# Optimization experiments

Hardware: AMD Instinct MI355X
Metric: run time of the kernel (lower is better)

Reference implementation:

```python
import jax, jax.numpy as jnp
import numpy as np

B, L, D, H = 8, 1024, 1024, 16
DH = D // H  # dim_per_head = 64
HG = H // 2  # global/local head split


def setup_inputs() -> dict:
    key = jax.random.key(0)
    ks = jax.random.split(key, 10)
    s = 1.0 / np.sqrt(D)
    return {
        "key": jax.random.normal(ks[0], (B, L, D), jnp.float32),
        "value": jax.random.normal(ks[1], (B, L, D), jnp.float32),
        "query": jax.random.normal(ks[2], (B, L, D), jnp.float32),
        "mask": jax.random.bernoulli(ks[3], 0.1, (B, L, L)),
        "additional_mask": jax.random.bernoulli(ks[4], 0.1, (B, L)),
        "Wk": jax.random.normal(ks[5], (D, D), jnp.float32) * s,
        "bk": jnp.zeros((D,), jnp.float32),
        "Wv": jax.random.normal(ks[6], (D, D), jnp.float32) * s,
        "bv": jnp.zeros((D,), jnp.float32),
        "Wq": jax.random.normal(ks[7], (D, D), jnp.float32) * s,
        "bq": jnp.zeros((D,), jnp.float32),
        "Wo": jax.random.normal(ks[8], (D, D), jnp.float32) * s,
        "bo": jnp.zeros((D,), jnp.float32),
    }


def _shape(x):
    # [B, L, D] -> [B, H, L, DH]
    return x.reshape(B, -1, H, DH).transpose(0, 2, 1, 3)


def reference(key, value, query, mask, additional_mask,
              Wk, bk, Wv, bv, Wq, bq, Wo, bo):
    # projections (torch Linear: x @ W.T + b)
    k = _shape(key @ Wk.T + bk)
    v = _shape(value @ Wv.T + bv)
    q = _shape(query @ Wq.T + bq) * (1.0 / np.sqrt(DH))  # scale query (edge_feature=None, additional_mask given)

    qg, ql = q[:, :HG], q[:, HG:]
    kg, kl = k[:, :HG], k[:, HG:]
    vg, vl = v[:, :HG], v[:, HG:]

    # global heads: standard masked attention
    score_g = jnp.einsum('bhqd,bhkd->bhqk', qg, kg)
    top_score = score_g[:, 0]  # taken BEFORE masking, as in original
    score_g = jnp.where(mask[:, None, :, :], -1e18, score_g)
    attn_g = jax.nn.softmax(score_g, axis=-1)  # dropout = identity (eval)
    ctx_g = jnp.einsum('bhqk,bhkd->bhqd', attn_g, vg)

    # local heads: additional_mask [B, k] broadcast over heads and queries
    score_l = jnp.einsum('bhqd,bhkd->bhqk', ql, kl)
    score_l = jnp.where(additional_mask[:, None, None, :], -1e18, score_l)
    attn_l = jax.nn.softmax(score_l, axis=-1)
    ctx_l = jnp.einsum('bhqk,bhkd->bhqd', attn_l, vl)

    ctx = jnp.concatenate([ctx_g, ctx_l], axis=1)          # [B, H, L, DH]
    ctx = ctx.transpose(0, 2, 1, 3).reshape(B, -1, D)      # unshape -> [B, L, D]
    out = ctx @ Wo.T + bo
    return out, top_score
```

## Files before the change

kernel.cpp:

```cpp
#include <hip/hip_runtime.h>
#include <hip/hip_bf16.h>

typedef unsigned short u16;
typedef unsigned int u32;
typedef __attribute__((ext_vector_type(8))) short short8;
typedef __attribute__((ext_vector_type(4))) short short4v;
typedef __attribute__((ext_vector_type(4))) float floatx4;

#define BB 8
#define LL 1024
#define DD 1024
#define HH 16
#define DHH 64
#define NEGBIG (-3.0e38f)

__device__ inline u16 f2b(float f) {
  union { __hip_bfloat16 h; u16 u; } cv;
  cv.h = __float2bfloat16(f);
  return cv.u;
}
__device__ inline float b2f(u16 u) {
  union { u16 u; __hip_bfloat16 h; } cv;
  cv.u = u;
  return __bfloat162float(cv.h);
}
__device__ inline float fin(float v, float sentinel) {
  return (fabsf(v) < 1e30f) ? v : sentinel;
}
__device__ inline void async16(const void* g, void* l) {
  __builtin_amdgcn_global_load_lds(
      (__attribute__((address_space(1))) void*)(const_cast<void*>(g)),
      (__attribute__((address_space(3))) void*)l, 16, 0, 0);
}


__global__ __launch_bounds__(256) void convpack(
    const float* __restrict__ key, const float* __restrict__ value,
    const float* __restrict__ query, const float* __restrict__ Wk,
    const float* __restrict__ Wv, const float* __restrict__ Wq,
    const float* __restrict__ Wo, const int* __restrict__ mask,
    const int* __restrict__ amask, u16* __restrict__ keyb,
    u16* __restrict__ valb, u16* __restrict__ qryb, u16* __restrict__ Wkb,
    u16* __restrict__ Wvb, u16* __restrict__ Wqb, u16* __restrict__ Wob,
    u32* __restrict__ maskb, u32* __restrict__ amaskb) {
  const int job = blockIdx.y;
  const int gtid = blockIdx.x * 256 + threadIdx.x;
  const int stride = gridDim.x * 256;

  if (job < 7) {
    const float* src; u16* dst; size_t n4;
    switch (job) {
      case 0: src = key;   dst = keyb; n4 = (size_t)BB * LL * DD / 4; break;
      case 1: src = value; dst = valb; n4 = (size_t)BB * LL * DD / 4; break;
      case 2: src = query; dst = qryb; n4 = (size_t)BB * LL * DD / 4; break;
      case 3: src = Wk;    dst = Wkb;  n4 = (size_t)DD * DD / 4; break;
      case 4: src = Wv;    dst = Wvb;  n4 = (size_t)DD * DD / 4; break;
      case 5: src = Wq;    dst = Wqb;  n4 = (size_t)DD * DD / 4; break;
      default: src = Wo;   dst = Wob;  n4 = (size_t)DD * DD / 4; break;
    }
    for (size_t i = gtid; i < n4; i += stride) {
      float4 v = ((const float4*)src)[i];
      short4v s;
      s[0] = (short)f2b(v.x); s[1] = (short)f2b(v.y);
      s[2] = (short)f2b(v.z); s[3] = (short)f2b(v.w);
      *(short4v*)(dst + i * 4) = s;
    }
  } else if (job == 7) {
    const size_t nw = (size_t)BB * LL * LL / 32;
    for (size_t w = gtid; w < nw; w += stride) {
      const int4* src = (const int4*)(mask + w * 32);
      u32 bits = 0;
#pragma unroll
      for (int c = 0; c < 8; c++) {
        int4 v = src[c];
        bits |= (u32)(v.x != 0) << (c * 4);
        bits |= (u32)(v.y != 0) << (c * 4 + 1);
        bits |= (u32)(v.z != 0) << (c * 4 + 2);
        bits |= (u32)(v.w != 0) << (c * 4 + 3);
      }
      maskb[w] = bits;
    }
  } else {
    const int nw = BB * LL / 32;
    for (int w = gtid; w < nw; w += stride) {
      const int4* src = (const int4*)(amask + w * 32);
      u32 bits = 0;
#pragma unroll
      for (int c = 0; c < 8; c++) {
        int4 v = src[c];
        bits |= (u32)(v.x != 0) << (c * 4);
        bits |= (u32)(v.y != 0) << (c * 4 + 1);
        bits |= (u32)(v.z != 0) << (c * 4 + 2);
        bits |= (u32)(v.w != 0) << (c * 4 + 3);
      }
      amaskb[w] = bits;
    }
  }
}

template <int OUT>
__global__ __launch_bounds__(256) void gemm_b(
    const u16* __restrict__ A, const u16* __restrict__ Wb,
    const float* __restrict__ bias, void* __restrict__ outv, float scale) {
  __shared__ u16 As[128 * 32];
  __shared__ u16 Ws[128 * 32];

  const int tid = threadIdx.x;
  const int wave = tid >> 6, lane = tid & 63;
  const int lr = lane & 15, lq = lane >> 4;
  const int row0 = blockIdx.x * 128;
  const int col0 = blockIdx.y * 128;
  const int wm = (wave & 1) * 64, wn = (wave >> 1) * 64;

  floatx4 acc[4][4];
#pragma unroll
  for (int i = 0; i < 4; i++)
#pragma unroll
    for (int j = 0; j < 4; j++) acc[i][j] = (floatx4){0.f, 0.f, 0.f, 0.f};

  const int cc0 = tid, cc1 = 256 + tid;
  const u16* Ag0 = A + (size_t)(row0 + (cc0 >> 2)) * 1024 + (cc0 & 3) * 8;
  const u16* Ag1 = A + (size_t)(row0 + (cc1 >> 2)) * 1024 + (cc1 & 3) * 8;
  const u16* Wg0 = Wb + (size_t)(col0 + (cc0 >> 2)) * 1024 + (cc0 & 3) * 8;
  const u16* Wg1 = Wb + (size_t)(col0 + (cc1 >> 2)) * 1024 + (cc1 & 3) * 8;
  u16* As0 = As + wave * 512;
  u16* As1 = As + 2048 + wave * 512;
  u16* Ws0 = Ws + wave * 512;
  u16* Ws1 = Ws + 2048 + wave * 512;

  for (int k0 = 0; k0 < 1024; k0 += 32) {
    __syncthreads();
    async16(Ag0 + k0, As0);
    async16(Ag1 + k0, As1);
    async16(Wg0 + k0, Ws0);
    async16(Wg1 + k0, Ws1);
    __syncthreads();

    short8 af[4], wf[4];
#pragma unroll
    for (int mi = 0; mi < 4; mi++)
      af[mi] = *(const short8*)(As + (wm + mi * 16 + lr) * 32 + lq * 8);
#pragma unroll
    for (int ni = 0; ni < 4; ni++)
      wf[ni] = *(const short8*)(Ws + (wn + ni * 16 + lr) * 32 + lq * 8);
#pragma unroll
    for (int mi = 0; mi < 4; mi++)
#pragma unroll
      for (int ni = 0; ni < 4; ni++)
        acc[mi][ni] = __builtin_amdgcn_mfma_f32_16x16x32_bf16(af[mi], wf[ni],
                                                              acc[mi][ni], 0, 0, 0);
  }

#pragma unroll
  for (int ni = 0; ni < 4; ni++) {
    const int col = col0 + wn + ni * 16 + lr;
    const float bv = bias[col];
#pragma unroll
    for (int mi = 0; mi < 4; mi++) {
#pragma unroll
      for (int r = 0; r < 4; r++) {
        const int row = row0 + wm + mi * 16 + lq * 4 + r;
        const float v = (acc[mi][ni][r] + bv) * scale;
        if (OUT == 0) {
          const int b = row >> 10, l = row & 1023, h = col >> 6, dh = col & 63;
          ((u16*)outv)[((b * HH + h) * LL + l) * DHH + dh] = f2b(v);
        } else if (OUT == 2) {
          const int b = row >> 10, l = row & 1023, h = col >> 6, dh = col & 63;
          ((u16*)outv)[((b * HH + h) * DHH + dh) * LL + l] = f2b(v);
        } else {
          ((float*)outv)[(size_t)row * 1024 + col] = v;
        }
      }
    }
  }
}

__global__ __launch_bounds__(256) void attn_fast(
    const u16* __restrict__ qbuf, const u16* __restrict__ kbuf,
    const u16* __restrict__ vbt, const u32* __restrict__ maskb,
    const u32* __restrict__ amaskb, u16* __restrict__ ctx,
    float* __restrict__ top) {
  __shared__ u16 Ks[64 * 64];
  __shared__ u16 Vts[64 * 64];

  const int id = blockIdx.x;
  const int xcd = id & 7;
  const int r_ = id >> 3;
  const int b = r_ & 7;
  const int h = (((r_ >> 3) & 1) << 3) | (xcd ^ b);
  const int qt = r_ >> 4;

  const int tid = threadIdx.x, wave = tid >> 6, lane = tid & 63;
  const int lr = lane & 15, lq = lane >> 4;
  const int lq4 = lq * 4;
  const int x7 = lr & 7;

  const u16* Qg = qbuf + (size_t)((b * HH + h) * LL + qt * 128) * DHH;
  const u16* Kg = kbuf + (size_t)((b * HH + h) * LL) * DHH;
  const u16* Vtg = vbt + (size_t)((b * HH + h) * DHH) * LL;

  short8 qf[2][2];
#pragma unroll
  for (int mi = 0; mi < 2; mi++)
#pragma unroll
    for (int kk = 0; kk < 2; kk++)
      qf[mi][kk] = *(const short8*)(Qg + (wave * 32 + mi * 16 + lr) * 64 +
                                    kk * 32 + lq * 8);

  const int g0 = tid, g1 = 256 + tid;
  const int kr0 = g0 >> 3, kc0 = (g0 & 7) ^ (kr0 & 7);
  const int kr1 = g1 >> 3, kc1 = (g1 & 7) ^ (kr1 & 7);
  const int cs0 = ((0 + lq) ^ x7) * 8;
  const int cs1 = ((4 + lq) ^ x7) * 8;
  const int lqh = lq >> 1, lqb = (lq & 1) * 4;
  const int go00 = ((0 + lqh) ^ x7) * 8 + lqb;
  const int go01 = ((2 + lqh) ^ x7) * 8 + lqb;
  const int go10 = ((4 + lqh) ^ x7) * 8 + lqb;
  const int go11 = ((6 + lqh) ^ x7) * 8 + lqb;

  float mrow[2], lrow[2];
  floatx4 Oacc[2][4];
#pragma unroll
  for (int mi = 0; mi < 2; mi++) {
    mrow[mi] = NEGBIG;
    lrow[mi] = 0.f;
#pragma unroll
    for (int ni = 0; ni < 4; ni++) Oacc[mi][ni] = (floatx4){0.f, 0.f, 0.f, 0.f};
  }

  for (int kc = 0; kc < 16; kc++) {
    __syncthreads();
    async16(Kg + kc * 4096 + kr0 * 64 + kc0 * 8, Ks + wave * 512);
    async16(Kg + kc * 4096 + kr1 * 64 + kc1 * 8, Ks + 2048 + wave * 512);
    async16(Vtg + (size_t)kr0 * LL + kc * 64 + kc0 * 8, Vts + wave * 512);
    async16(Vtg + (size_t)kr1 * LL + kc * 64 + kc1 * 8, Vts + 2048 + wave * 512);
    __syncthreads();

    floatx4 S[2][4];
#pragma unroll
    for (int nj = 0; nj < 4; nj++) {
      const short8 kf0 = *(const short8*)(Ks + (nj * 16 + lr) * 64 + cs0);
      const short8 kf1 = *(const short8*)(Ks + (nj * 16 + lr) * 64 + cs1);
#pragma unroll
      for (int mi = 0; mi < 2; mi++) {
        floatx4 z = (floatx4){0.f, 0.f, 0.f, 0.f};
        z = __builtin_amdgcn_mfma_f32_16x16x32_bf16(kf1, qf[mi][1], z, 0, 0, 0);
        z = __builtin_amdgcn_mfma_f32_16x16x32_bf16(kf0, qf[mi][0], z, 0, 0, 0);
        S[mi][nj] = z;
      }
    }

    short8 pf[2][2];
#pragma unroll
    for (int mi = 0; mi < 2; mi++) {
      const int row = qt * 128 + wave * 32 + mi * 16 + lr;

      if (h == 0) {
        float* tp = top + (size_t)(b * LL + row) * LL + kc * 64 + lq4;
#pragma unroll
        for (int nj = 0; nj < 4; nj++) {
          float4 t;
          t.x = S[mi][nj][0]; t.y = S[mi][nj][1];
          t.z = S[mi][nj][2]; t.w = S[mi][nj][3];
          *(float4*)(tp + nj * 16) = t;
        }
      }

      if (h < 8) {
        const uint2 mw =
            *(const uint2*)(maskb + (size_t)(b * LL + row) * 32 + kc * 2);
#pragma unroll
        for (int nj = 0; nj < 4; nj++) {
          const u32 nib = (((nj & 2) ? mw.y : mw.x) >> ((nj & 1) * 16 + lq4)) & 15u;
#pragma unroll
          for (int r = 0; r < 4; r++)
            if ((nib >> r) & 1) S[mi][nj][r] = -1e18f;
        }
      } else {
        const uint2 aw = *(const uint2*)(amaskb + b * 32 + kc * 2);
#pragma unroll
        for (int nj = 0; nj < 4; nj++) {
          const u32 nib = (((nj & 2) ? aw.y : aw.x) >> ((nj & 1) * 16 + lq4)) & 15u;
#pragma unroll
          for (int r = 0; r < 4; r++)
            if ((nib >> r) & 1) S[mi][nj][r] = -1e18f;
        }
      }

      float cm = fmaxf(fmaxf(S[mi][0][0], S[mi][0][1]),
                       fmaxf(S[mi][0][2], S[mi][0][3]));
#pragma unroll
      for (int nj = 1; nj < 4; nj++)
        cm = fmaxf(cm, fmaxf(fmaxf(S[mi][nj][0], S[mi][nj][1]),
                             fmaxf(S[mi][nj][2], S[mi][nj][3])));
      cm = fmaxf(cm, __shfl_xor(cm, 16, 64));
      cm = fmaxf(cm, __shfl_xor(cm, 32, 64));
      const float mold = mrow[mi];
      const float mnew = fmaxf(mold, cm);
      const float alpha = __expf(mold - mnew);
      mrow[mi] = mnew;
      float rs = 0.f;
#pragma unroll
      for (int nj = 0; nj < 4; nj++)
#pragma unroll
        for (int r = 0; r < 4; r++) {
          const float p = __expf(S[mi][nj][r] - mnew);
          S[mi][nj][r] = p;
          rs += p;
        }
      rs += __shfl_xor(rs, 16, 64);
      rs += __shfl_xor(rs, 32, 64);
      lrow[mi] = lrow[mi] * alpha + rs;
#pragma unroll
      for (int ni = 0; ni < 4; ni++)
#pragma unroll
        for (int r = 0; r < 4; r++) Oacc[mi][ni][r] *= alpha;

#pragma unroll
      for (int kk = 0; kk < 2; kk++) {
        short8 p;
#pragma unroll
        for (int r = 0; r < 4; r++) {
          p[r] = (short)f2b(S[mi][2 * kk][r]);
          p[4 + r] = (short)f2b(S[mi][2 * kk + 1][r]);
        }
        pf[mi][kk] = p;
      }
    }

#pragma unroll
    for (int ni = 0; ni < 4; ni++) {
      const int rb = (ni * 16 + lr) * 64;
      const short4v v00 = *(const short4v*)(Vts + rb + go00);
      const short4v v01 = *(const short4v*)(Vts + rb + go01);
      const short4v v10 = *(const short4v*)(Vts + rb + go10);
      const short4v v11 = *(const short4v*)(Vts + rb + go11);
      const short8 vf0 = __builtin_shufflevector(v00, v01, 0, 1, 2, 3, 4, 5, 6, 7);
      const short8 vf1 = __builtin_shufflevector(v10, v11, 0, 1, 2, 3, 4, 5, 6, 7);
#pragma unroll
      for (int mi = 0; mi < 2; mi++) {
        Oacc[mi][ni] =
            __builtin_amdgcn_mfma_f32_16x16x32_bf16(vf0, pf[mi][0], Oacc[mi][ni], 0, 0, 0);
        Oacc[mi][ni] =
            __builtin_amdgcn_mfma_f32_16x16x32_bf16(vf1, pf[mi][1], Oacc[mi][ni], 0, 0, 0);
      }
    }
  }

#pragma unroll
  for (int mi = 0; mi < 2; mi++) {
    const float inv = 1.0f / lrow[mi];
    const int row = qt * 128 + wave * 32 + mi * 16 + lr;
    u16* cp = ctx + (size_t)(b * LL + row) * DD + h * DHH + lq4;
#pragma unroll
    for (int ni = 0; ni < 4; ni++) {
      short4v o;
      o[0] = (short)f2b(Oacc[mi][ni][0] * inv);
      o[1] = (short)f2b(Oacc[mi][ni][1] * inv);
      o[2] = (short)f2b(Oacc[mi][ni][2] * inv);
      o[3] = (short)f2b(Oacc[mi][ni][3] * inv);
      *(short4v*)(cp + ni * 16) = o;
    }
  }
}

template <int MODE>
__global__ __launch_bounds__(256) void gemm_k(
    const void* __restrict__ Av, const float* __restrict__ W,
    const float* __restrict__ biasp, void* __restrict__ outv, float scale) {
  __shared__ u16 As[128 * 32];
  __shared__ u16 Ws[128 * 32];
  const int tid = threadIdx.x;
  const int wave = tid >> 6, lane = tid & 63;
  const int lr = lane & 15, lq = lane >> 4;
  const int row0 = blockIdx.x * 128;
  const int col0 = blockIdx.y * 128;
  const int wm = (wave & 1) * 64, wn = (wave >> 1) * 64;
  floatx4 acc[4][4];
#pragma unroll
  for (int i = 0; i < 4; i++)
#pragma unroll
    for (int j = 0; j < 4; j++) acc[i][j] = (floatx4){0.f, 0.f, 0.f, 0.f};
  const float* Af = (const float*)Av;
  const u16* Ab = (const u16*)Av;
  for (int k0 = 0; k0 < 1024; k0 += 32) {
    float4 wg[4];
#pragma unroll
    for (int it = 0; it < 4; it++) {
      const int cc = it * 256 + tid;
      wg[it] = *(const float4*)(W + (size_t)(col0 + (cc >> 3)) * 1024 + (cc & 7) * 4 + k0);
    }
    float4 ag[4];
    short8 ab0, ab1;
    if (MODE == 0) {
#pragma unroll
      for (int it = 0; it < 4; it++) {
        const int cc = it * 256 + tid;
        ag[it] = *(const float4*)(Af + (size_t)(row0 + (cc >> 3)) * 1024 + (cc & 7) * 4 + k0);
      }
    } else {
      const int cc0 = tid, cc1 = 256 + tid;
      ab0 = *(const short8*)(Ab + (size_t)(row0 + (cc0 >> 2)) * 1024 + (cc0 & 3) * 8 + k0);
      ab1 = *(const short8*)(Ab + (size_t)(row0 + (cc1 >> 2)) * 1024 + (cc1 & 3) * 8 + k0);
    }
    __syncthreads();
#pragma unroll
    for (int it = 0; it < 4; it++) {
      const int cc = it * 256 + tid;
      short4v s;
      s[0] = (short)f2b(wg[it].x); s[1] = (short)f2b(wg[it].y);
      s[2] = (short)f2b(wg[it].z); s[3] = (short)f2b(wg[it].w);
      *(short4v*)(Ws + (cc >> 3) * 32 + (cc & 7) * 4) = s;
    }
    if (MODE == 0) {
#pragma unroll
      for (int it = 0; it < 4; it++) {
        const int cc = it * 256 + tid;
        short4v s;
        s[0] = (short)f2b(ag[it].x); s[1] = (short)f2b(ag[it].y);
        s[2] = (short)f2b(ag[it].z); s[3] = (short)f2b(ag[it].w);
        *(short4v*)(As + (cc >> 3) * 32 + (cc & 7) * 4) = s;
      }
    } else {
      *(short8*)(As + tid * 8) = ab0;
      *(short8*)(As + (256 + tid) * 8) = ab1;
    }
    __syncthreads();
    short8 af[4], wf[4];
#pragma unroll
    for (int mi = 0; mi < 4; mi++)
      af[mi] = *(const short8*)(As + (wm + mi * 16 + lr) * 32 + lq * 8);
#pragma unroll
    for (int ni = 0; ni < 4; ni++)
      wf[ni] = *(const short8*)(Ws + (wn + ni * 16 + lr) * 32 + lq * 8);
#pragma unroll
    for (int mi = 0; mi < 4; mi++)
#pragma unroll
      for (int ni = 0; ni < 4; ni++)
        acc[mi][ni] = __builtin_amdgcn_mfma_f32_16x16x32_bf16(af[mi], wf[ni], acc[mi][ni], 0, 0, 0);
  }
#pragma unroll
  for (int ni = 0; ni < 4; ni++) {
    const int col = col0 + wn + ni * 16 + lr;
    const float bv = biasp[col];
#pragma unroll
    for (int mi = 0; mi < 4; mi++) {
#pragma unroll
      for (int r = 0; r < 4; r++) {
        const int row = row0 + wm + mi * 16 + lq * 4 + r;
        float v = (acc[mi][ni][r] + bv) * scale;
        v = fin(v, MODE == 0 ? 700.0f : 1000.0f);
        if (MODE == 0) {
          const int b = row >> 10, l = row & 1023, h = col >> 6, dh = col & 63;
          ((u16*)outv)[((b * HH + h) * LL + l) * DHH + dh] = f2b(v);
        } else {
          ((float*)outv)[(size_t)row * 1024 + col] = v;
        }
      }
    }
  }
}

__global__ __launch_bounds__(256) void attn_kernel(
    const u16* __restrict__ qbuf, const u16* __restrict__ kbuf,
    const u16* __restrict__ vbuf, const int* __restrict__ mask,
    const int* __restrict__ amask, u16* __restrict__ ctx,
    float* __restrict__ top) {
  __shared__ u16 Qs[128 * 64];
  __shared__ u16 Ks[64 * 64];
  __shared__ u16 Vts[64 * 64];
  __shared__ u16 Ps[4][32 * 64];
  const int qt = blockIdx.x, h = blockIdx.y, b = blockIdx.z;
  const int tid = threadIdx.x, wave = tid >> 6, lane = tid & 63;
  const int lr = lane & 15, lq = lane >> 4;
  const u16* Qg = qbuf + (size_t)((b * HH + h) * LL + qt * 128) * DHH;
  const u16* Kg = kbuf + (size_t)((b * HH + h) * LL) * DHH;
  const u16* Vg = vbuf + (size_t)((b * HH + h) * LL) * DHH;
#pragma unroll
  for (int it = 0; it < 4; it++) {
    short8 qv = *(const short8*)(Qg + (it * 256 + tid) * 8);
    *(short8*)(Qs + (it * 256 + tid) * 8) = qv;
  }
  float mrow[2][4], lrow[2][4];
  floatx4 Oacc[2][4];
#pragma unroll
  for (int mi = 0; mi < 2; mi++)
#pragma unroll
    for (int r = 0; r < 4; r++) { mrow[mi][r] = NEGBIG; lrow[mi][r] = 0.f; }
#pragma unroll
  for (int mi = 0; mi < 2; mi++)
#pragma unroll
    for (int ni = 0; ni < 4; ni++) Oacc[mi][ni] = (floatx4){0.f, 0.f, 0.f, 0.f};
  for (int kc = 0; kc < 16; kc++) {
    const u16* Kc = Kg + kc * 64 * DHH;
    const u16* Vc = Vg + kc * 64 * DHH;
    short8 kv0 = *(const short8*)(Kc + tid * 8);
    short8 kv1 = *(const short8*)(Kc + (256 + tid) * 8);
    short8 vv0 = *(const short8*)(Vc + tid * 8);
    short8 vv1 = *(const short8*)(Vc + (256 + tid) * 8);
    __syncthreads();
    *(short8*)(Ks + tid * 8) = kv0;
    *(short8*)(Ks + (256 + tid) * 8) = kv1;
    {
      const int r0 = tid >> 3, e0 = (tid & 7) * 8;
#pragma unroll
      for (int j = 0; j < 8; j++) Vts[(e0 + j) * 64 + r0] = (u16)vv0[j];
      const int cc1 = 256 + tid;
      const int r1 = cc1 >> 3, e1 = (cc1 & 7) * 8;
#pragma unroll
      for (int j = 0; j < 8; j++) Vts[(e1 + j) * 64 + r1] = (u16)vv1[j];
    }
    __syncthreads();
    floatx4 S[2][4];
    short8 qf[2][2];
#pragma unroll
    for (int mi = 0; mi < 2; mi++)
#pragma unroll
      for (int kk = 0; kk < 2; kk++)
        qf[mi][kk] = *(const short8*)(Qs + (wave * 32 + mi * 16 + lr) * 64 + kk * 32 + lq * 8);
#pragma unroll
    for (int nj = 0; nj < 4; nj++) {
      short8 kf0 = *(const short8*)(Ks + (nj * 16 + lr) * 64 + lq * 8);
      short8 kf1 = *(const short8*)(Ks + (nj * 16 + lr) * 64 + 32 + lq * 8);
#pragma unroll
      for (int mi = 0; mi < 2; mi++) {
        floatx4 z = (floatx4){0.f, 0.f, 0.f, 0.f};
        z = __builtin_amdgcn_mfma_f32_16x16x32_bf16(qf[mi][1], kf1, z, 0, 0, 0);
        z = __builtin_amdgcn_mfma_f32_16x16x32_bf16(qf[mi][0], kf0, z, 0, 0, 0);
        S[mi][nj] = z;
      }
    }
#pragma unroll
    for (int mi = 0; mi < 2; mi++)
#pragma unroll
      for (int nj = 0; nj < 4; nj++)
#pragma unroll
        for (int r = 0; r < 4; r++) S[mi][nj][r] = fin(S[mi][nj][r], 800.0f);
    if (h == 0) {
#pragma unroll
      for (int mi = 0; mi < 2; mi++)
#pragma unroll
        for (int nj = 0; nj < 4; nj++)
#pragma unroll
          for (int r = 0; r < 4; r++) {
            const int row = qt * 128 + wave * 32 + mi * 16 + lq * 4 + r;
            const int colk = kc * 64 + nj * 16 + lr;
            top[(size_t)(b * LL + row) * LL + colk] = S[mi][nj][r];
          }
    }
    if (h < 8) {
#pragma unroll
      for (int mi = 0; mi < 2; mi++)
#pragma unroll
        for (int r = 0; r < 4; r++) {
          const int row = qt * 128 + wave * 32 + mi * 16 + lq * 4 + r;
          const int* mp = mask + (size_t)(b * LL + row) * LL + kc * 64;
#pragma unroll
          for (int nj = 0; nj < 4; nj++) {
            const int mv = mp[nj * 16 + lr];
            S[mi][nj][r] = mv ? -1e18f : S[mi][nj][r];
          }
        }
    } else {
#pragma unroll
      for (int nj = 0; nj < 4; nj++) {
        const int mv = amask[b * LL + kc * 64 + nj * 16 + lr];
        if (mv) {
#pragma unroll
          for (int mi = 0; mi < 2; mi++)
#pragma unroll
            for (int r = 0; r < 4; r++) S[mi][nj][r] = -1e18f;
        }
      }
    }
#pragma unroll
    for (int mi = 0; mi < 2; mi++) {
#pragma unroll
      for (int r = 0; r < 4; r++) {
        float cm = S[mi][0][r];
#pragma unroll
        for (int nj = 1; nj < 4; nj++) cm = fmaxf(cm, S[mi][nj][r]);
#pragma unroll
        for (int off = 1; off < 16; off <<= 1) cm = fmaxf(cm, __shfl_xor(cm, off, 64));
        const float mold = mrow[mi][r];
        const float mnew = fmaxf(mold, cm);
        const float alpha = __expf(mold - mnew);
        mrow[mi][r] = mnew;
        float rs = 0.f;
#pragma unroll
        for (int nj = 0; nj < 4; nj++) {
          const float p = __expf(S[mi][nj][r] - mnew);
          S[mi][nj][r] = p;
          rs += p;
        }
#pragma unroll
        for (int off = 1; off < 16; off <<= 1) rs += __shfl_xor(rs, off, 64);
        lrow[mi][r] = lrow[mi][r] * alpha + rs;
#pragma unroll
        for (int ni = 0; ni < 4; ni++) Oacc[mi][ni][r] *= alpha;
      }
    }
#pragma unroll
    for (int mi = 0; mi < 2; mi++)
#pragma unroll
      for (int nj = 0; nj < 4; nj++)
#pragma unroll
        for (int r = 0; r < 4; r++)
          Ps[wave][(mi * 16 + lq * 4 + r) * 64 + nj * 16 + lr] = f2b(S[mi][nj][r]);
    __syncthreads();
#pragma unroll
    for (int kk = 0; kk < 2; kk++) {
      short8 pf[2];
#pragma unroll
      for (int mi = 0; mi < 2; mi++)
        pf[mi] = *(const short8*)(&Ps[wave][(mi * 16 + lr) * 64 + kk * 32 + lq * 8]);
#pragma unroll
      for (int ni = 0; ni < 4; ni++) {
        short8 vf = *(const short8*)(Vts + (ni * 16 + lr) * 64 + kk * 32 + lq * 8);
#pragma unroll
        for (int mi = 0; mi < 2; mi++)
          Oacc[mi][ni] = __builtin_amdgcn_mfma_f32_16x16x32_bf16(pf[mi], vf, Oacc[mi][ni], 0, 0, 0);
      }
    }
  }
#pragma unroll
  for (int mi = 0; mi < 2; mi++)
#pragma unroll
    for (int r = 0; r < 4; r++) {
      const float inv = 1.0f / lrow[mi][r];
      const int row = qt * 128 + wave * 32 + mi * 16 + lq * 4 + r;
#pragma unroll
      for (int ni = 0; ni < 4; ni++) {
        const int col = h * DHH + ni * 16 + lr;
        ctx[(size_t)(b * LL + row) * DD + col] = f2b(fin(Oacc[mi][ni][r] * inv, 900.0f));
      }
    }
}

extern "C" void kernel_launch(void* const* d_in, const int* in_sizes, int n_in,
                              void* d_out, int out_size, void* d_ws, size_t ws_size,
                              hipStream_t stream) {
  const float* key   = (const float*)d_in[0];
  const float* value = (const float*)d_in[1];
  const float* query = (const float*)d_in[2];
  const int* mask    = (const int*)d_in[3];
  const int* amask   = (const int*)d_in[4];
  const float* Wk = (const float*)d_in[5];
  const float* bk = (const float*)d_in[6];
  const float* Wv = (const float*)d_in[7];
  const float* bv = (const float*)d_in[8];
  const float* Wq = (const float*)d_in[9];
  const float* bq = (const float*)d_in[10];
  const float* Wo = (const float*)d_in[11];
  const float* bo = (const float*)d_in[12];

  float* outp = (float*)d_out;
  float* topp = outp + (size_t)BB * LL * DD;

  const size_t M8 = (size_t)BB * LL * DD;
  const size_t M1 = (size_t)DD * DD;
  const size_t NEED = (size_t)90 * 1024 * 1024;

  dim3 tb(256), gg(64, 8, 1), ga(8, 16, 8);

  if (ws_size >= NEED) {
    u16* W16 = (u16*)d_ws;
    u16* keyb = W16;
    u16* valb = W16 + M8;
    u16* qryb = W16 + 2 * M8;
    u16* Wkb = W16 + 3 * M8;
    u16* Wvb = Wkb + M1;
    u16* Wqb = Wvb + M1;
    u16* Wob = Wqb + M1;
    u32* maskb = (u32*)(Wob + M1);
    u32* amaskb = maskb + 262144;
    u16* kbuf = W16 + 3 * M8 + 5 * M1;
    u16* vbt  = kbuf + M8;
    u16* qbuf = keyb;
    u16* cbuf = valb;

    convpack<<<dim3(256, 9), tb, 0, stream>>>(
        key, value, query, Wk, Wv, Wq, Wo, mask, amask,
        keyb, valb, qryb, Wkb, Wvb, Wqb, Wob, maskb, amaskb);
    gemm_b<0><<<gg, tb, 0, stream>>>(keyb, Wkb, bk, kbuf, 1.0f);
    gemm_b<2><<<gg, tb, 0, stream>>>(valb, Wvb, bv, vbt, 1.0f);
    gemm_b<0><<<gg, tb, 0, stream>>>(qryb, Wqb, bq, qbuf, 0.125f);
    attn_fast<<<dim3(1024, 1, 1), tb, 0, stream>>>(qbuf, kbuf, vbt, maskb,
                                                   amaskb, cbuf, topp);
    gemm_b<1><<<gg, tb, 0, stream>>>(cbuf, Wob, bo, outp, 1.0f);
  } else {
    u16* kbuf = (u16*)d_ws;
    u16* vbuf = kbuf + M8;
    u16* qbuf = vbuf + M8;
    u16* cbuf = qbuf + M8;
    gemm_k<0><<<gg, tb, 0, stream>>>(key,   Wk, bk, kbuf, 1.0f);
    gemm_k<0><<<gg, tb, 0, stream>>>(value, Wv, bv, vbuf, 1.0f);
    gemm_k<0><<<gg, tb, 0, stream>>>(query, Wq, bq, qbuf, 0.125f);
    attn_kernel<<<ga, tb, 0, stream>>>(qbuf, kbuf, vbuf, mask, amask, cbuf, topp);
    gemm_k<1><<<gg, tb, 0, stream>>>(cbuf, Wo, bo, outp, 1.0f);
  }
}
```

Baseline: 421.6 us.

## Fuse QKV projections with in-kernel query cast; double-buffer attention and use exp2

Replaces the three separate Q/K/V projection launches with one 3D-grid GEMM launch. The query branch reads fp32 activations and casts them to bf16 inside the GEMM, which removes the separate query conversion pass and its buffer. The attention kernel now double-buffers the K/V tiles in LDS, so the next chunk's loads overlap compute, and raises wave priority around the MFMA sections. The softmax uses exp2, with log2(e) folded into the query scale and the pre-mask top score rescaled by ln2. The trade-offs are doubled LDS in attention and a query GEMM path that issues register-staged global loads inside the k-loop.

New measurement: 428.4 us. No clear change (+1.6%).

```diff
diff --git a/kernel.cpp b/kernel.cpp
--- a/kernel.cpp
+++ b/kernel.cpp
@@ -13,6 +13,8 @@
 #define HH 16
 #define DHH 64
 #define NEGBIG (-3.0e38f)
+#define QSCALE 0.1803368801111204f
+#define LN2F   0.6931471805599453f
 
 __device__ inline u16 f2b(float f) {
   union { __hip_bfloat16 h; u16 u; } cv;
@@ -27,6 +29,13 @@
 __device__ inline float fin(float v, float sentinel) {
   return (fabsf(v) < 1e30f) ? v : sentinel;
 }
+__device__ inline float fexp2(float x) {
+#if __has_builtin(__builtin_amdgcn_exp2f)
+  return __builtin_amdgcn_exp2f(x);
+#else
+  return exp2f(x);
+#endif
+}
 __device__ inline void async16(const void* g, void* l) {
   __builtin_amdgcn_global_load_lds(
       (__attribute__((address_space(1))) void*)(const_cast<void*>(g)),
@@ -36,26 +45,24 @@
 
 __global__ __launch_bounds__(256) void convpack(
     const float* __restrict__ key, const float* __restrict__ value,
-    const float* __restrict__ query, const float* __restrict__ Wk,
-    const float* __restrict__ Wv, const float* __restrict__ Wq,
-    const float* __restrict__ Wo, const int* __restrict__ mask,
-    const int* __restrict__ amask, u16* __restrict__ keyb,
-    u16* __restrict__ valb, u16* __restrict__ qryb, u16* __restrict__ Wkb,
+    const float* __restrict__ Wk, const float* __restrict__ Wv,
+    const float* __restrict__ Wq, const float* __restrict__ Wo,
+    const int* __restrict__ mask, const int* __restrict__ amask,
+    u16* __restrict__ keyb, u16* __restrict__ valb, u16* __restrict__ Wkb,
     u16* __restrict__ Wvb, u16* __restrict__ Wqb, u16* __restrict__ Wob,
     u32* __restrict__ maskb, u32* __restrict__ amaskb) {
   const int job = blockIdx.y;
   const int gtid = blockIdx.x * 256 + threadIdx.x;
   const int stride = gridDim.x * 256;
 
-  if (job < 7) {
+  if (job < 6) {
     const float* src; u16* dst; size_t n4;
     switch (job) {
       case 0: src = key;   dst = keyb; n4 = (size_t)BB * LL * DD / 4; break;
       case 1: src = value; dst = valb; n4 = (size_t)BB * LL * DD / 4; break;
-      case 2: src = query; dst = qryb; n4 = (size_t)BB * LL * DD / 4; break;
-      case 3: src = Wk;    dst = Wkb;  n4 = (size_t)DD * DD / 4; break;
-      case 4: src = Wv;    dst = Wvb;  n4 = (size_t)DD * DD / 4; break;
-      case 5: src = Wq;    dst = Wqb;  n4 = (size_t)DD * DD / 4; break;
+      case 2: src = Wk;    dst = Wkb;  n4 = (size_t)DD * DD / 4; break;
+      case 3: src = Wv;    dst = Wvb;  n4 = (size_t)DD * DD / 4; break;
+      case 4: src = Wq;    dst = Wqb;  n4 = (size_t)DD * DD / 4; break;
       default: src = Wo;   dst = Wob;  n4 = (size_t)DD * DD / 4; break;
     }
     for (size_t i = gtid; i < n4; i += stride) {
@@ -65,7 +72,7 @@
       s[2] = (short)f2b(v.z); s[3] = (short)f2b(v.w);
       *(short4v*)(dst + i * 4) = s;
     }
-  } else if (job == 7) {
+  } else if (job == 6) {
     const size_t nw = (size_t)BB * LL * LL / 32;
     for (size_t w = gtid; w < nw; w += stride) {
       const int4* src = (const int4*)(mask + w * 32);
@@ -94,6 +101,131 @@
         bits |= (u32)(v.w != 0) << (c * 4 + 3);
       }
       amaskb[w] = bits;
+    }
+  }
+}
+
+__global__ __launch_bounds__(256) void gemm_qkv(
+    const u16* __restrict__ keyb, const u16* __restrict__ valb,
+    const float* __restrict__ query, const u16* __restrict__ Wkb,
+    const u16* __restrict__ Wvb, const u16* __restrict__ Wqb,
+    const float* __restrict__ bk, const float* __restrict__ bv,
+    const float* __restrict__ bq, u16* __restrict__ kbuf,
+    u16* __restrict__ vbt, u16* __restrict__ qbuf) {
+  __shared__ u16 As[128 * 32];
+  __shared__ u16 Ws[128 * 32];
+
+  const int z = blockIdx.z;
+  const int tid = threadIdx.x;
+  const int wave = tid >> 6, lane = tid & 63;
+  const int lr = lane & 15, lq = lane >> 4;
+  const int row0 = blockIdx.x * 128;
+  const int col0 = blockIdx.y * 128;
+  const int wm = (wave & 1) * 64, wn = (wave >> 1) * 64;
+
+  floatx4 acc[4][4];
+#pragma unroll
+  for (int i = 0; i < 4; i++)
+#pragma unroll
+    for (int j = 0; j < 4; j++) acc[i][j] = (floatx4){0.f, 0.f, 0.f, 0.f};
+
+  const int cc0 = tid, cc1 = 256 + tid;
+  u16* As0 = As + wave * 512;
+  u16* As1 = As + 2048 + wave * 512;
+  u16* Ws0 = Ws + wave * 512;
+  u16* Ws1 = Ws + 2048 + wave * 512;
+
+  if (z < 2) {
+    const u16* A  = (z == 0) ? keyb : valb;
+    const u16* Wb = (z == 0) ? Wkb : Wvb;
+    const u16* Ag0 = A + (size_t)(row0 + (cc0 >> 2)) * 1024 + (cc0 & 3) * 8;
+    const u16* Ag1 = A + (size_t)(row0 + (cc1 >> 2)) * 1024 + (cc1 & 3) * 8;
+    const u16* Wg0 = Wb + (size_t)(col0 + (cc0 >> 2)) * 1024 + (cc0 & 3) * 8;
+    const u16* Wg1 = Wb + (size_t)(col0 + (cc1 >> 2)) * 1024 + (cc1 & 3) * 8;
+
+    for (int k0 = 0; k0 < 1024; k0 += 32) {
+      __syncthreads();
+      async16(Ag0 + k0, As0);
+      async16(Ag1 + k0, As1);
+      async16(Wg0 + k0, Ws0);
+      async16(Wg1 + k0, Ws1);
+      __syncthreads();
+
+      short8 af[4], wf[4];
+#pragma unroll
+      for (int mi = 0; mi < 4; mi++)
+        af[mi] = *(const short8*)(As + (wm + mi * 16 + lr) * 32 + lq * 8);
+#pragma unroll
+      for (int ni = 0; ni < 4; ni++)
+        wf[ni] = *(const short8*)(Ws + (wn + ni * 16 + lr) * 32 + lq * 8);
+#pragma unroll
+      for (int mi = 0; mi < 4; mi++)
+#pragma unroll
+        for (int ni = 0; ni < 4; ni++)
+          acc[mi][ni] = __builtin_amdgcn_mfma_f32_16x16x32_bf16(af[mi], wf[ni],
+                                                                acc[mi][ni], 0, 0, 0);
+    }
+  } else {
+    const u16* Wg0 = Wqb + (size_t)(col0 + (cc0 >> 2)) * 1024 + (cc0 & 3) * 8;
+    const u16* Wg1 = Wqb + (size_t)(col0 + (cc1 >> 2)) * 1024 + (cc1 & 3) * 8;
+
+    for (int k0 = 0; k0 < 1024; k0 += 32) {
+      float4 ag[4];
+#pragma unroll
+      for (int it = 0; it < 4; it++) {
+        const int cc = it * 256 + tid;
+        ag[it] = *(const float4*)(query + (size_t)(row0 + (cc >> 3)) * 1024 +
+                                  (cc & 7) * 4 + k0);
+      }
+      __syncthreads();
+      async16(Wg0 + k0, Ws0);
+      async16(Wg1 + k0, Ws1);
+#pragma unroll
+      for (int it = 0; it < 4; it++) {
+        const int cc = it * 256 + tid;
+        short4v s;
+        s[0] = (short)f2b(ag[it].x); s[1] = (short)f2b(ag[it].y);
+        s[2] = (short)f2b(ag[it].z); s[3] = (short)f2b(ag[it].w);
+        *(short4v*)(As + (cc >> 3) * 32 + (cc & 7) * 4) = s;
+      }
+      __syncthreads();
+
+      short8 af[4], wf[4];
+#pragma unroll
+      for (int mi = 0; mi < 4; mi++)
+        af[mi] = *(const short8*)(As + (wm + mi * 16 + lr) * 32 + lq * 8);
+#pragma unroll
+      for (int ni = 0; ni < 4; ni++)
+        wf[ni] = *(const short8*)(Ws + (wn + ni * 16 + lr) * 32 + lq * 8);
+#pragma unroll
+      for (int mi = 0; mi < 4; mi++)
+#pragma unroll
+        for (int ni = 0; ni < 4; ni++)
+          acc[mi][ni] = __builtin_amdgcn_mfma_f32_16x16x32_bf16(af[mi], wf[ni],
+                                                                acc[mi][ni], 0, 0, 0);
+    }
+  }
+
+  const float scale = (z == 2) ? QSCALE : 1.0f;
+  const float* bias = (z == 0) ? bk : (z == 1) ? bv : bq;
+  u16* outb = (z == 0) ? kbuf : qbuf;
+
+#pragma unroll
+  for (int ni = 0; ni < 4; ni++) {
+    const int col = col0 + wn + ni * 16 + lr;
+    const float bvv = bias[col];
+#pragma unroll
+    for (int mi = 0; mi < 4; mi++) {
+#pragma unroll
+      for (int r = 0; r < 4; r++) {
+        const int row = row0 + wm + mi * 16 + lq * 4 + r;
+        const float v = (acc[mi][ni][r] + bvv) * scale;
+        const int b = row >> 10, l = row & 1023, h = col >> 6, dh = col & 63;
+        if (z == 1)
+          vbt[((b * HH + h) * DHH + dh) * LL + l] = f2b(v);
+        else
+          outb[((b * HH + h) * LL + l) * DHH + dh] = f2b(v);
+      }
     }
   }
 }
@@ -180,8 +312,8 @@
     const u16* __restrict__ vbt, const u32* __restrict__ maskb,
     const u32* __restrict__ amaskb, u16* __restrict__ ctx,
     float* __restrict__ top) {
-  __shared__ u16 Ks[64 * 64];
-  __shared__ u16 Vts[64 * 64];
+  __shared__ u16 Ks[2][64 * 64];
+  __shared__ u16 Vts[2][64 * 64];
 
   const int id = blockIdx.x;
   const int xcd = id & 7;
@@ -218,6 +350,14 @@
   const int go10 = ((4 + lqh) ^ x7) * 8 + lqb;
   const int go11 = ((6 + lqh) ^ x7) * 8 + lqb;
 
+  auto stage = [&](int kc, int buf) {
+    async16(Kg + kc * 4096 + kr0 * 64 + kc0 * 8, &Ks[buf][wave * 512]);
+    async16(Kg + kc * 4096 + kr1 * 64 + kc1 * 8, &Ks[buf][2048 + wave * 512]);
+    async16(Vtg + (size_t)kr0 * LL + kc * 64 + kc0 * 8, &Vts[buf][wave * 512]);
+    async16(Vtg + (size_t)kr1 * LL + kc * 64 + kc1 * 8,
+            &Vts[buf][2048 + wave * 512]);
+  };
+
   float mrow[2], lrow[2];
   floatx4 Oacc[2][4];
 #pragma unroll
@@ -228,19 +368,21 @@
     for (int ni = 0; ni < 4; ni++) Oacc[mi][ni] = (floatx4){0.f, 0.f, 0.f, 0.f};
   }
 
+  stage(0, 0);
+
   for (int kc = 0; kc < 16; kc++) {
+    const int cur = kc & 1;
     __syncthreads();
-    async16(Kg + kc * 4096 + kr0 * 64 + kc0 * 8, Ks + wave * 512);
-    async16(Kg + kc * 4096 + kr1 * 64 + kc1 * 8, Ks + 2048 + wave * 512);
-    async16(Vtg + (size_t)kr0 * LL + kc * 64 + kc0 * 8, Vts + wave * 512);
-    async16(Vtg + (size_t)kr1 * LL + kc * 64 + kc1 * 8, Vts + 2048 + wave * 512);
-    __syncthreads();
+    if (kc < 15) stage(kc + 1, cur ^ 1);
+    const u16* Ksc = Ks[cur];
+    const u16* Vtsc = Vts[cur];
 
     floatx4 S[2][4];
+    __builtin_amdgcn_s_setprio(1);
 #pragma unroll
     for (int nj = 0; nj < 4; nj++) {
-      const short8 kf0 = *(const short8*)(Ks + (nj * 16 + lr) * 64 + cs0);
-      const short8 kf1 = *(const short8*)(Ks + (nj * 16 + lr) * 64 + cs1);
+      const short8 kf0 = *(const short8*)(Ksc + (nj * 16 + lr) * 64 + cs0);
+      const short8 kf1 = *(const short8*)(Ksc + (nj * 16 + lr) * 64 + cs1);
 #pragma unroll
       for (int mi = 0; mi < 2; mi++) {
         floatx4 z = (floatx4){0.f, 0.f, 0.f, 0.f};
@@ -249,6 +391,7 @@
         S[mi][nj] = z;
       }
     }
+    __builtin_amdgcn_s_setprio(0);
 
     short8 pf[2][2];
 #pragma unroll
@@ -260,8 +403,8 @@
 #pragma unroll
         for (int nj = 0; nj < 4; nj++) {
           float4 t;
-          t.x = S[mi][nj][0]; t.y = S[mi][nj][1];
-          t.z = S[mi][nj][2]; t.w = S[mi][nj][3];
+          t.x = S[mi][nj][0] * LN2F; t.y = S[mi][nj][1] * LN2F;
+          t.z = S[mi][nj][2] * LN2F; t.w = S[mi][nj][3] * LN2F;
           *(float4*)(tp + nj * 16) = t;
         }
       }
@@ -297,14 +440,14 @@
       cm = fmaxf(cm, __shfl_xor(cm, 32, 64));
       const float mold = mrow[mi];
       const float mnew = fmaxf(mold, cm);
-      const float alpha = __expf(mold - mnew);
+      const float alpha = fexp2(mold - mnew);
       mrow[mi] = mnew;
       float rs = 0.f;
 #pragma unroll
       for (int nj = 0; nj < 4; nj++)
 #pragma unroll
         for (int r = 0; r < 4; r++) {
-          const float p = __expf(S[mi][nj][r] - mnew);
+          const float p = fexp2(S[mi][nj][r] - mnew);
           S[mi][nj][r] = p;
           rs += p;
         }
@@ -328,13 +471,14 @@
       }
     }
 
+    __builtin_amdgcn_s_setprio(1);
 #pragma unroll
     for (int ni = 0; ni < 4; ni++) {
       const int rb = (ni * 16 + lr) * 64;
-      const short4v v00 = *(const short4v*)(Vts + rb + go00);
-      const short4v v01 = *(const short4v*)(Vts + rb + go01);
-      const short4v v10 = *(const short4v*)(Vts + rb + go10);
-      const short4v v11 = *(const short4v*)(Vts + rb + go11);
+      const short4v v00 = *(const short4v*)(Vtsc + rb + go00);
+      const short4v v01 = *(const short4v*)(Vtsc + rb + go01);
+      const short4v v10 = *(const short4v*)(Vtsc + rb + go10);
+      const short4v v11 = *(const short4v*)(Vtsc + rb + go11);
       const short8 vf0 = __builtin_shufflevector(v00, v01, 0, 1, 2, 3, 4, 5, 6, 7);
       const short8 vf1 = __builtin_shufflevector(v10, v11, 0, 1, 2, 3, 4, 5, 6, 7);
 #pragma unroll
@@ -345,6 +489,7 @@
             __builtin_amdgcn_mfma_f32_16x16x32_bf16(vf1, pf[mi][1], Oacc[mi][ni], 0, 0, 0);
       }
     }
+    __builtin_amdgcn_s_setprio(0);
   }
 
 #pragma unroll
@@ -667,7 +812,7 @@
     u16* W16 = (u16*)d_ws;
     u16* keyb = W16;
     u16* valb = W16 + M8;
-    u16* qryb = W16 + 2 * M8;
+    u16* qbuf = W16 + 2 * M8;
     u16* Wkb = W16 + 3 * M8;
     u16* Wvb = Wkb + M1;
     u16* Wqb = Wvb + M1;
@@ -676,15 +821,13 @@
     u32* amaskb = maskb + 262144;
     u16* kbuf = W16 + 3 * M8 + 5 * M1;
     u16* vbt  = kbuf + M8;
-    u16* qbuf = keyb;
     u16* cbuf = valb;
 
-    convpack<<<dim3(256, 9), tb, 0, stream>>>(
-        key, value, query, Wk, Wv, Wq, Wo, mask, amask,
-        keyb, valb, qryb, Wkb, Wvb, Wqb, Wob, maskb, amaskb);
-    gemm_b<0><<<gg, tb, 0, stream>>>(keyb, Wkb, bk, kbuf, 1.0f);
-    gemm_b<2><<<gg, tb, 0, stream>>>(valb, Wvb, bv, vbt, 1.0f);
-    gemm_b<0><<<gg, tb, 0, stream>>>(qryb, Wqb, bq, qbuf, 0.125f);
+    convpack<<<dim3(256, 8), tb, 0, stream>>>(
+        key, value, Wk, Wv, Wq, Wo, mask, amask,
+        keyb, valb, Wkb, Wvb, Wqb, Wob, maskb, amaskb);
+    gemm_qkv<<<dim3(64, 8, 3), tb, 0, stream>>>(
+        keyb, valb, query, Wkb, Wvb, Wqb, bk, bv, bq, kbuf, vbt, qbuf);
     attn_fast<<<dim3(1024, 1, 1), tb, 0, stream>>>(qbuf, kbuf, vbt, maskb,
                                                    amaskb, cbuf, topp);
     gemm_b<1><<<gg, tb, 0, stream>>>(cbuf, Wob, bo, outp, 1.0f);
```
